# Optimization experiments

Hardware: AMD Instinct MI355X
Metric: run time of the kernel (lower is better)

The kernel has to match this reference:

```python
import jax, jax.numpy as jnp
import numpy as np

N = 100000   # nodes
E = 1600000  # edges (avg degree 16)
F = 128      # num_features
H = 128      # hidden_channels
C = 8        # num_classes


def _gcn_conv(x, src, dst, W, b, num_nodes):
    """PyG GCNConv: add self-loops, symmetric normalization, linear-then-aggregate, +bias."""
    h = x @ W  # [N, out]
    loops = jnp.arange(num_nodes, dtype=src.dtype)
    s = jnp.concatenate([src, loops])
    d = jnp.concatenate([dst, loops])
    deg = jax.ops.segment_sum(jnp.ones_like(s, dtype=h.dtype), d, num_segments=num_nodes)
    dinv = jax.lax.rsqrt(jnp.maximum(deg, 1.0))  # deg >= 1 thanks to self-loops
    norm = dinv[s] * dinv[d]  # [E+N]
    out = jax.ops.segment_sum(h[s] * norm[:, None], d, num_segments=num_nodes)
    return out + b


def setup_inputs() -> dict:
    key = jax.random.key(0)
    k1, k2, k3, k4 = jax.random.split(key, 4)
    x = jax.random.normal(k1, (N, F), dtype=jnp.float32)
    edge_index = jax.random.randint(k2, (2, E), 0, N, dtype=jnp.int32)
    W1 = jax.random.normal(k3, (F, H), dtype=jnp.float32) * (1.0 / np.sqrt(F))
    b1 = jnp.zeros((H,), dtype=jnp.float32)
    W2 = jax.random.normal(k4, (H, C), dtype=jnp.float32) * (1.0 / np.sqrt(H))
    b2 = jnp.zeros((C,), dtype=jnp.float32)
    return {"x": x, "edge_index": edge_index, "W1": W1, "b1": b1, "W2": W2, "b2": b2}


def reference(x, edge_index, W1, b1, W2, b2):
    src, dst = edge_index[0], edge_index[1]
    h = _gcn_conv(x, src, dst, W1, b1, N)
    h = jax.nn.relu(h)
    out = _gcn_conv(h, src, dst, W2, b2, N)
    return out
```

## Files before the change

### kernel.cpp

```cpp
#include <hip/hip_runtime.h>
#include <hip/hip_bf16.h>
#include <hip/hip_fp16.h>

#define NN 100000
#define EE 1600000
#define FF 128
#define HH 128
#define CC 8

#define CH 8192
#define NBK ((NN + 255) / 256)
#define NCH ((EE + CH - 1) / CH)
#define HSZ (NBK * NCH)

typedef _Float16 half8 __attribute__((ext_vector_type(8)));
typedef float f32x4 __attribute__((ext_vector_type(4)));

__global__ __launch_bounds__(1024) void k_scan1(const int* __restrict__ in,
                                                int* __restrict__ outp,
                                                int* __restrict__ bsum, int n) {
  __shared__ int sh[1024];
  int t = threadIdx.x;
  int i = blockIdx.x * 1024 + t;
  int v = (i < n) ? in[i] : 0;
  sh[t] = v;
  __syncthreads();
  for (int offs = 1; offs < 1024; offs <<= 1) {
    int add = (t >= offs) ? sh[t - offs] : 0;
    __syncthreads();
    sh[t] += add;
    __syncthreads();
  }
  if (i < n) outp[i] = sh[t] - v;
  if (t == 1023) bsum[blockIdx.x] = sh[1023];
}

__global__ __launch_bounds__(256) void k_scan2(int* __restrict__ bsum, int nb) {
  __shared__ int sh[256];
  int t = threadIdx.x;
  int v = (t < nb) ? bsum[t] : 0;
  sh[t] = v;
  __syncthreads();
  for (int offs = 1; offs < 256; offs <<= 1) {
    int add = (t >= offs) ? sh[t - offs] : 0;
    __syncthreads();
    sh[t] += add;
    __syncthreads();
  }
  if (t < nb) bsum[t] = sh[t] - v;
}

__global__ __launch_bounds__(256) void k_histA(const int* __restrict__ dst,
                                               int* __restrict__ hist) {
  __shared__ int lh[NBK];
  int c = blockIdx.x, t = threadIdx.x;
  for (int b = t; b < NBK; b += 256) lh[b] = 0;
  __syncthreads();
  int e0 = c * CH, e1 = min(e0 + CH, EE);
  for (int j = e0 + t; j < e1; j += 256) atomicAdd(&lh[dst[j] >> 8], 1);
  __syncthreads();
  for (int b = t; b < NBK; b += 256) hist[b * NCH + c] = lh[b];
}

__global__ __launch_bounds__(256) void k_scat_gemm1(
    const int* __restrict__ src, const int* __restrict__ dst,
    const int* __restrict__ hist_s, const int* __restrict__ bsum,
    unsigned int* __restrict__ stage,
    const float* __restrict__ x, const float* __restrict__ W,
    __half* __restrict__ h, int n) {
  __shared__ _Float16 Wl[128 * 128];
  int t = threadIdx.x;

  if (blockIdx.x < NCH) {
    int* lcur = (int*)Wl;
    int c = blockIdx.x;
    for (int b = t; b < NBK; b += 256) {
      int idx = b * NCH + c;
      lcur[b] = hist_s[idx] + bsum[idx >> 10];
    }
    __syncthreads();
    int e0 = c * CH, e1 = min(e0 + CH, EE);
    for (int j = e0 + t; j < e1; j += 256) {
      int d = dst[j];
      int pos = atomicAdd(&lcur[d >> 8], 1);
      stage[pos] = (unsigned int)src[j] | ((unsigned int)(d & 255) << 17);
    }
    return;
  }

  {
    int c = t & 127;
    int kg0 = t >> 7;
    for (int kg = kg0; kg < 16; kg += 2) {
      _Float16 tmp[8];
#pragma unroll
      for (int j = 0; j < 8; ++j)
        tmp[j] = (_Float16)W[(size_t)(kg * 8 + j) * 128 + c];
      int byteoff = (c * 256 + kg * 16) ^ ((c & 7) << 4);
      *(half8*)((char*)Wl + byteoff) = *(half8*)tmp;
    }
  }
  __syncthreads();

  int row0 = (blockIdx.x - NCH) * 64;
  int w = t >> 6, l = t & 63;
  int rw = w >> 1, cw = w & 1;
  int lr = l & 15, g = l >> 4;

  f32x4 acc[2][4];
#pragma unroll
  for (int ar = 0; ar < 2; ++ar)
#pragma unroll
    for (int bt = 0; bt < 4; ++bt)
#pragma unroll
      for (int r = 0; r < 4; ++r) acc[ar][bt][r] = 0.f;

  for (int kt = 0; kt < 4; ++kt) {
    half8 a[2];
#pragma unroll
    for (int ar = 0; ar < 2; ++ar) {
      int row = row0 + rw * 32 + ar * 16 + lr;
      if (row < n) {
        const float* p = &x[(size_t)row * 128 + kt * 32 + g * 8];
        float4 v0 = *(const float4*)p;
        float4 v1 = *(const float4*)(p + 4);
        a[ar][0] = (_Float16)v0.x; a[ar][1] = (_Float16)v0.y;
        a[ar][2] = (_Float16)v0.z; a[ar][3] = (_Float16)v0.w;
        a[ar][4] = (_Float16)v1.x; a[ar][5] = (_Float16)v1.y;
        a[ar][6] = (_Float16)v1.z; a[ar][7] = (_Float16)v1.w;
      } else {
#pragma unroll
        for (int j = 0; j < 8; ++j) a[ar][j] = (_Float16)0.f;
      }
    }
#pragma unroll
    for (int bt = 0; bt < 4; ++bt) {
      int c = cw * 64 + bt * 16 + lr;
      int byteoff = (c * 256 + kt * 64 + g * 16) ^ ((c & 7) << 4);
      half8 bb = *(const half8*)((const char*)Wl + byteoff);
      acc[0][bt] = __builtin_amdgcn_mfma_f32_16x16x32_f16(a[0], bb, acc[0][bt], 0, 0, 0);
      acc[1][bt] = __builtin_amdgcn_mfma_f32_16x16x32_f16(a[1], bb, acc[1][bt], 0, 0, 0);
    }
  }

#pragma unroll
  for (int ar = 0; ar < 2; ++ar)
#pragma unroll
    for (int bt = 0; bt < 4; ++bt)
#pragma unroll
      for (int r = 0; r < 4; ++r) {
        int row = row0 + rw * 32 + ar * 16 + g * 4 + r;
        int c = cw * 64 + bt * 16 + lr;
        if (row < n) h[(size_t)row * 128 + c] = __float2half(acc[ar][bt][r]);
      }
}

__global__ __launch_bounds__(256) void k_bucketB(const unsigned int* __restrict__ stage,
                                                 const int* __restrict__ hist_s,
                                                 const int* __restrict__ bsum,
                                                 int* __restrict__ col,
                                                 int* __restrict__ rowptr,
                                                 float* __restrict__ dinv) {
  __shared__ int lcnt[256];
  __shared__ int lpart[256];
  int b = blockIdx.x, t = threadIdx.x;
  int n0 = b * 256;
  lcnt[t] = 0;
  int i0 = b * NCH;
  int e0 = hist_s[i0] + bsum[i0 >> 10];
  int e1;
  if (b == NBK - 1) {
    e1 = EE;
  } else {
    int i1 = (b + 1) * NCH;
    e1 = hist_s[i1] + bsum[i1 >> 10];
  }
  __syncthreads();
  for (int j = e0 + t; j < e1; j += 256)
    atomicAdd(&lcnt[stage[j] >> 17], 1);
  __syncthreads();
  int c = lcnt[t];
  lpart[t] = c;
  __syncthreads();
  for (int offs = 1; offs < 256; offs <<= 1) {
    int add = (t >= offs) ? lpart[t - offs] : 0;
    __syncthreads();
    lpart[t] += add;
    __syncthreads();
  }
  int base = e0 + lpart[t] - c;
  int node = n0 + t;
  if (node <= NN) rowptr[node] = base;
  if (node < NN) dinv[node] = rsqrtf((float)c + 1.f);
  __syncthreads();
  lcnt[t] = base;
  __syncthreads();
  for (int j = e0 + t; j < e1; j += 256) {
    unsigned int v = stage[j];
    int pos = atomicAdd(&lcnt[v >> 17], 1);
    col[pos] = (int)(v & 0x1FFFFu);
  }
}

__global__ __launch_bounds__(256) void k_agg1g(const __half* __restrict__ h,
                                               const int* __restrict__ rowptr,
                                               const int* __restrict__ col,
                                               const float* __restrict__ dinv,
                                               const float* __restrict__ b1,
                                               const float* __restrict__ W2,
                                               __half* __restrict__ h2, int n) {
  __shared__ float arow[4][128];
  int wid = threadIdx.x >> 6;
  int lane = threadIdx.x & 63;
  int node = blockIdx.x * 4 + wid;
  if (node >= n) return;
  float dn = dinv[node];
  const __half2* hp = (const __half2*)h;
  float2 acc = make_float2(0.f, 0.f);
  int e0 = rowptr[node], e1 = rowptr[node + 1];
  int e = e0;
  for (; e + 7 < e1; e += 8) {
    int s[8];
#pragma unroll
    for (int u = 0; u < 8; ++u) s[u] = col[e + u];
    float w[8];
    __half2 f[8];
#pragma unroll
    for (int u = 0; u < 8; ++u) w[u] = dinv[s[u]];
#pragma unroll
    for (int u = 0; u < 8; ++u) f[u] = hp[(size_t)s[u] * 64 + lane];
#pragma unroll
    for (int u = 0; u < 8; ++u) {
      float2 ff = __half22float2(f[u]);
      float ww = w[u] * dn;
      acc.x = fmaf(ww, ff.x, acc.x);
      acc.y = fmaf(ww, ff.y, acc.y);
    }
  }
  for (; e + 1 < e1; e += 2) {
    int s0 = col[e], s1 = col[e + 1];
    float w0 = dinv[s0] * dn, w1 = dinv[s1] * dn;
    float2 f0 = __half22float2(hp[(size_t)s0 * 64 + lane]);
    float2 f1 = __half22float2(hp[(size_t)s1 * 64 + lane]);
    acc.x = fmaf(w0, f0.x, acc.x); acc.y = fmaf(w0, f0.y, acc.y);
    acc.x = fmaf(w1, f1.x, acc.x); acc.y = fmaf(w1, f1.y, acc.y);
  }
  if (e < e1) {
    int s = col[e];
    float w = dinv[s] * dn;
    float2 f = __half22float2(hp[(size_t)s * 64 + lane]);
    acc.x = fmaf(w, f.x, acc.x);
    acc.y = fmaf(w, f.y, acc.y);
  }
  {
    float w = dn * dn;
    float2 f = __half22float2(hp[(size_t)node * 64 + lane]);
    acc.x = fmaf(w, f.x, acc.x);
    acc.y = fmaf(w, f.y, acc.y);
  }
  float2 bb = ((const float2*)b1)[lane];
  acc.x = fmaxf(acc.x + bb.x, 0.f);
  acc.y = fmaxf(acc.y + bb.y, 0.f);

  *(float2*)&arow[wid][2 * lane] = acc;
  asm volatile("" ::: "memory");
  int colc = lane & 7;
  int kg = lane >> 3;
  float p = 0.f;
#pragma unroll
  for (int j = 0; j < 16; ++j) {
    int k = kg * 16 + j;
    p = fmaf(arow[wid][k], W2[k * 8 + colc], p);
  }
  p += __shfl_xor(p, 8);
  p += __shfl_xor(p, 16);
  p += __shfl_xor(p, 32);
  if (lane < 8) h2[(size_t)node * 8 + colc] = __float2half(p);
}

__global__ __launch_bounds__(256) void k_agg2(const __half* __restrict__ h2,
                                              const int* __restrict__ rowptr,
                                              const int* __restrict__ col,
                                              const float* __restrict__ dinv,
                                              const float* __restrict__ b2,
                                              float* __restrict__ out, int n) {
  int gthread = blockIdx.x * 256 + threadIdx.x;
  int node = gthread >> 3, f = gthread & 7;
  if (node >= n) return;
  float dn = dinv[node];
  float acc = 0.f;
  int e0 = rowptr[node], e1 = rowptr[node + 1];
  int e = e0;
  for (; e + 7 < e1; e += 8) {
    int s[8];
#pragma unroll
    for (int u = 0; u < 8; ++u) s[u] = col[e + u];
    float w[8];
    float v[8];
#pragma unroll
    for (int u = 0; u < 8; ++u) w[u] = dinv[s[u]];
#pragma unroll
    for (int u = 0; u < 8; ++u) v[u] = __half2float(h2[(size_t)s[u] * 8 + f]);
#pragma unroll
    for (int u = 0; u < 8; ++u) acc = fmaf(w[u] * dn, v[u], acc);
  }
  for (; e < e1; ++e) {
    int s = col[e];
    acc = fmaf(dinv[s] * dn, __half2float(h2[(size_t)s * 8 + f]), acc);
  }
  acc = fmaf(dn * dn, __half2float(h2[(size_t)node * 8 + f]), acc);
  out[(size_t)node * 8 + f] = acc + b2[f];
}

extern "C" void kernel_launch(void* const* d_in, const int* in_sizes, int n_in,
                              void* d_out, int out_size, void* d_ws, size_t ws_size,
                              hipStream_t stream) {
  const float* x  = (const float*)d_in[0];
  const int* eidx = (const int*)d_in[1];
  const float* W1 = (const float*)d_in[2];
  const float* b1 = (const float*)d_in[3];
  const float* W2 = (const float*)d_in[4];
  const float* b2 = (const float*)d_in[5];
  float* out = (float*)d_out;
  const int* src = eidx;
  const int* dst = eidx + EE;

  char* ws = (char*)d_ws;
  size_t off = 0;
  auto alloc = [&](size_t bytes) -> char* {
    char* p = ws + off;
    off = (off + bytes + 255) & ~(size_t)255;
    return p;
  };

  float*        dinv   = (float*)       alloc((size_t)NN * 4);
  int*          rowptr = (int*)         alloc((size_t)(NN + 1) * 4);
  int*          bsum   = (int*)         alloc(1024 * 4);
  int*          hist_g = (int*)         alloc((size_t)HSZ * 4);
  int*          hist_s = (int*)         alloc((size_t)HSZ * 4);
  unsigned int* stage  = (unsigned int*)alloc((size_t)EE * 4);
  int*          colbuf = (int*)         alloc((size_t)EE * 4);
  __half*       h1     = (__half*)      alloc((size_t)NN * HH * 2);
  __half*       h2     = (__half*)      alloc((size_t)NN * CC * 2);

  int nbScanH = (HSZ + 1023) / 1024;

  k_histA<<<NCH, 256, 0, stream>>>(dst, hist_g);
  k_scan1<<<nbScanH, 1024, 0, stream>>>(hist_g, hist_s, bsum, HSZ);
  k_scan2<<<1, 256, 0, stream>>>(bsum, nbScanH);

  int nbG1 = (NN + 63) / 64;
  k_scat_gemm1<<<NCH + nbG1, 256, 0, stream>>>(src, dst, hist_s, bsum, stage,
                                               x, W1, h1, NN);
  k_bucketB<<<NBK, 256, 0, stream>>>(stage, hist_s, bsum, colbuf, rowptr, dinv);

  k_agg1g<<<(NN + 3) / 4, 256, 0, stream>>>(h1, rowptr, colbuf, dinv, b1, W2,
                                            h2, NN);
  k_agg2<<<(NN * 8 + 255) / 256, 256, 0, stream>>>(h2, rowptr, colbuf, dinv,
                                                   b2, out, NN);
}
```

Before: 165.8 us.

## Split layer-2 GEMM out of aggregation and make GEMM1 blocks persistent

The GEMM1 part of the fused scatter/GEMM kernel now runs on a fixed 320 blocks that loop over row tiles, so W1 is staged into shared memory once per block rather than once per tile. The second-layer projection (128 to 8) is taken out of the aggregation kernel. Aggregation now writes the full ReLU'd 128-wide fp16 hidden rows to a new buffer, and a separate per-row GEMV kernel then computes h2, reusing the h1 buffer. This removes the shared-memory staging and shuffle reduction from the gather kernel, at the cost of writing and re-reading a 25.6 MB intermediate and one extra launch.

```diff
diff --git a/kernel.cpp b/kernel.cpp
--- a/kernel.cpp
+++ b/kernel.cpp
@@ -12,6 +12,8 @@
 #define NBK ((NN + 255) / 256)
 #define NCH ((EE + CH - 1) / CH)
 #define HSZ (NBK * NCH)
+#define NT ((NN + 63) / 64)
+#define G1B 320
 
 typedef _Float16 half8 __attribute__((ext_vector_type(8)));
 typedef float f32x4 __attribute__((ext_vector_type(4)));
@@ -102,57 +104,59 @@
   }
   __syncthreads();
 
-  int row0 = (blockIdx.x - NCH) * 64;
   int w = t >> 6, l = t & 63;
   int rw = w >> 1, cw = w & 1;
   int lr = l & 15, g = l >> 4;
 
-  f32x4 acc[2][4];
-#pragma unroll
-  for (int ar = 0; ar < 2; ++ar)
-#pragma unroll
-    for (int bt = 0; bt < 4; ++bt)
-#pragma unroll
-      for (int r = 0; r < 4; ++r) acc[ar][bt][r] = 0.f;
-
-  for (int kt = 0; kt < 4; ++kt) {
-    half8 a[2];
-#pragma unroll
-    for (int ar = 0; ar < 2; ++ar) {
-      int row = row0 + rw * 32 + ar * 16 + lr;
-      if (row < n) {
-        const float* p = &x[(size_t)row * 128 + kt * 32 + g * 8];
-        float4 v0 = *(const float4*)p;
-        float4 v1 = *(const float4*)(p + 4);
-        a[ar][0] = (_Float16)v0.x; a[ar][1] = (_Float16)v0.y;
-        a[ar][2] = (_Float16)v0.z; a[ar][3] = (_Float16)v0.w;
-        a[ar][4] = (_Float16)v1.x; a[ar][5] = (_Float16)v1.y;
-        a[ar][6] = (_Float16)v1.z; a[ar][7] = (_Float16)v1.w;
-      } else {
-#pragma unroll
-        for (int j = 0; j < 8; ++j) a[ar][j] = (_Float16)0.f;
+  for (int tile = blockIdx.x - NCH; tile < NT; tile += G1B) {
+    int row0 = tile * 64;
+    f32x4 acc[2][4];
+#pragma unroll
+    for (int ar = 0; ar < 2; ++ar)
+#pragma unroll
+      for (int bt = 0; bt < 4; ++bt)
+#pragma unroll
+        for (int r = 0; r < 4; ++r) acc[ar][bt][r] = 0.f;
+
+    for (int kt = 0; kt < 4; ++kt) {
+      half8 a[2];
+#pragma unroll
+      for (int ar = 0; ar < 2; ++ar) {
+        int row = row0 + rw * 32 + ar * 16 + lr;
+        if (row < n) {
+          const float* p = &x[(size_t)row * 128 + kt * 32 + g * 8];
+          float4 v0 = *(const float4*)p;
+          float4 v1 = *(const float4*)(p + 4);
+          a[ar][0] = (_Float16)v0.x; a[ar][1] = (_Float16)v0.y;
+          a[ar][2] = (_Float16)v0.z; a[ar][3] = (_Float16)v0.w;
+          a[ar][4] = (_Float16)v1.x; a[ar][5] = (_Float16)v1.y;
+          a[ar][6] = (_Float16)v1.z; a[ar][7] = (_Float16)v1.w;
+        } else {
+#pragma unroll
+          for (int j = 0; j < 8; ++j) a[ar][j] = (_Float16)0.f;
+        }
       }
-    }
-#pragma unroll
-    for (int bt = 0; bt < 4; ++bt) {
-      int c = cw * 64 + bt * 16 + lr;
-      int byteoff = (c * 256 + kt * 64 + g * 16) ^ ((c & 7) << 4);
-      half8 bb = *(const half8*)((const char*)Wl + byteoff);
-      acc[0][bt] = __builtin_amdgcn_mfma_f32_16x16x32_f16(a[0], bb, acc[0][bt], 0, 0, 0);
-      acc[1][bt] = __builtin_amdgcn_mfma_f32_16x16x32_f16(a[1], bb, acc[1][bt], 0, 0, 0);
-    }
-  }
-
-#pragma unroll
-  for (int ar = 0; ar < 2; ++ar)
-#pragma unroll
-    for (int bt = 0; bt < 4; ++bt)
-#pragma unroll
-      for (int r = 0; r < 4; ++r) {
-        int row = row0 + rw * 32 + ar * 16 + g * 4 + r;
+#pragma unroll
+      for (int bt = 0; bt < 4; ++bt) {
         int c = cw * 64 + bt * 16 + lr;
-        if (row < n) h[(size_t)row * 128 + c] = __float2half(acc[ar][bt][r]);
+        int byteoff = (c * 256 + kt * 64 + g * 16) ^ ((c & 7) << 4);
+        half8 bb = *(const half8*)((const char*)Wl + byteoff);
+        acc[0][bt] = __builtin_amdgcn_mfma_f32_16x16x32_f16(a[0], bb, acc[0][bt], 0, 0, 0);
+        acc[1][bt] = __builtin_amdgcn_mfma_f32_16x16x32_f16(a[1], bb, acc[1][bt], 0, 0, 0);
       }
+    }
+
+#pragma unroll
+    for (int ar = 0; ar < 2; ++ar)
+#pragma unroll
+      for (int bt = 0; bt < 4; ++bt)
+#pragma unroll
+        for (int r = 0; r < 4; ++r) {
+          int row = row0 + rw * 32 + ar * 16 + g * 4 + r;
+          int c = cw * 64 + bt * 16 + lr;
+          if (row < n) h[(size_t)row * 128 + c] = __float2half(acc[ar][bt][r]);
+        }
+  }
 }
 
 __global__ __launch_bounds__(256) void k_bucketB(const unsigned int* __restrict__ stage,
@@ -202,14 +206,12 @@
   }
 }
 
-__global__ __launch_bounds__(256) void k_agg1g(const __half* __restrict__ h,
-                                               const int* __restrict__ rowptr,
-                                               const int* __restrict__ col,
-                                               const float* __restrict__ dinv,
-                                               const float* __restrict__ b1,
-                                               const float* __restrict__ W2,
-                                               __half* __restrict__ h2, int n) {
-  __shared__ float arow[4][128];
+__global__ __launch_bounds__(256) void k_agg1(const __half* __restrict__ h,
+                                              const int* __restrict__ rowptr,
+                                              const int* __restrict__ col,
+                                              const float* __restrict__ dinv,
+                                              const float* __restrict__ b1,
+                                              __half2* __restrict__ out, int n) {
   int wid = threadIdx.x >> 6;
   int lane = threadIdx.x & 63;
   int node = blockIdx.x * 4 + wid;
@@ -261,21 +263,33 @@
   float2 bb = ((const float2*)b1)[lane];
   acc.x = fmaxf(acc.x + bb.x, 0.f);
   acc.y = fmaxf(acc.y + bb.y, 0.f);
-
-  *(float2*)&arow[wid][2 * lane] = acc;
-  asm volatile("" ::: "memory");
-  int colc = lane & 7;
-  int kg = lane >> 3;
-  float p = 0.f;
-#pragma unroll
-  for (int j = 0; j < 16; ++j) {
-    int k = kg * 16 + j;
-    p = fmaf(arow[wid][k], W2[k * 8 + colc], p);
-  }
-  p += __shfl_xor(p, 8);
-  p += __shfl_xor(p, 16);
-  p += __shfl_xor(p, 32);
-  if (lane < 8) h2[(size_t)node * 8 + colc] = __float2half(p);
+  out[(size_t)node * 64 + lane] = __floats2half2_rn(acc.x, acc.y);
+}
+
+__global__ __launch_bounds__(256) void k_gemm2(const __half* __restrict__ a,
+                                               const float* __restrict__ W2,
+                                               __half* __restrict__ h2, int n) {
+  int r = blockIdx.x * 256 + threadIdx.x;
+  if (r >= n) return;
+  float acc[8];
+#pragma unroll
+  for (int c = 0; c < 8; ++c) acc[c] = 0.f;
+  const __half2* ap = (const __half2*)(a + (size_t)r * 128);
+#pragma unroll 8
+  for (int k2 = 0; k2 < 64; ++k2) {
+    float2 v = __half22float2(ap[k2]);
+    int k = k2 * 2;
+#pragma unroll
+    for (int c = 0; c < 8; ++c) {
+      acc[c] = fmaf(v.x, W2[(k + 0) * 8 + c], acc[c]);
+      acc[c] = fmaf(v.y, W2[(k + 1) * 8 + c], acc[c]);
+    }
+  }
+  union { __half2 h2v[4]; uint4 u; } pk;
+#pragma unroll
+  for (int c = 0; c < 4; ++c)
+    pk.h2v[c] = __floats2half2_rn(acc[2 * c], acc[2 * c + 1]);
+  *(uint4*)&h2[(size_t)r * 8] = pk.u;
 }
 
 __global__ __launch_bounds__(256) void k_agg2(const __half* __restrict__ h2,
@@ -341,7 +355,8 @@
   unsigned int* stage  = (unsigned int*)alloc((size_t)EE * 4);
   int*          colbuf = (int*)         alloc((size_t)EE * 4);
   __half*       h1     = (__half*)      alloc((size_t)NN * HH * 2);
-  __half*       h2     = (__half*)      alloc((size_t)NN * CC * 2);
+  __half2*      agg1   = (__half2*)     alloc((size_t)NN * HH * 2);
+  __half*       h2     = (__half*)h1;
 
   int nbScanH = (HSZ + 1023) / 1024;
 
@@ -349,13 +364,12 @@
   k_scan1<<<nbScanH, 1024, 0, stream>>>(hist_g, hist_s, bsum, HSZ);
   k_scan2<<<1, 256, 0, stream>>>(bsum, nbScanH);
 
-  int nbG1 = (NN + 63) / 64;
-  k_scat_gemm1<<<NCH + nbG1, 256, 0, stream>>>(src, dst, hist_s, bsum, stage,
-                                               x, W1, h1, NN);
+  k_scat_gemm1<<<NCH + G1B, 256, 0, stream>>>(src, dst, hist_s, bsum, stage,
+                                              x, W1, h1, NN);
   k_bucketB<<<NBK, 256, 0, stream>>>(stage, hist_s, bsum, colbuf, rowptr, dinv);
 
-  k_agg1g<<<(NN + 3) / 4, 256, 0, stream>>>(h1, rowptr, colbuf, dinv, b1, W2,
-                                            h2, NN);
+  k_agg1<<<(NN + 3) / 4, 256, 0, stream>>>(h1, rowptr, colbuf, dinv, b1, agg1, NN);
+  k_gemm2<<<(NN + 255) / 256, 256, 0, stream>>>((const __half*)agg1, W2, h2, NN);
   k_agg2<<<(NN * 8 + 255) / 256, 256, 0, stream>>>(h2, rowptr, colbuf, dinv,
                                                    b2, out, NN);
 }
```

Measured after the change: 169.5 us. 1.02x slower.
